# Kernel tuning notes

Measured on AMD Instinct MI355X. Metric: run time of the kernel, lower is better.

Reference implementation:

```python
import jax, jax.numpy as jnp
import numpy as np

FP = 1e-4  # floating_point smoothing constant from the source


def setup_inputs() -> dict:
    key = jax.random.key(0)
    k1, k2 = jax.random.split(key)
    N, F, B = 100000, 50, 16
    x = jax.random.randint(k1, (N, F, B), 0, 2).astype(jnp.float32)  # 0/1 one-hot-style indicators
    y = jax.random.randint(k2, (N,), 0, 2).astype(jnp.int32)         # binary labels
    return {"x": x, "y": y}


def _wls_fit(X, pct, w):
    # X: [F,K,p] design, pct: [F,K] WLS weights, w: [F,K] targets
    XtW = jnp.swapaxes(X, 1, 2) * pct[:, None, :]           # [F,p,K] = X^T W (W diagonal)
    A = XtW @ X                                              # [F,p,p]
    coef = jnp.linalg.pinv(A) @ (XtW @ w[..., None])         # [F,p,1]
    fit = (X @ coef)[..., 0]                                 # [F,K]
    return fit, coef


def reference(x, y):
    N = x.shape[0]
    m1 = (y == 1).astype(x.dtype)                            # bad mask
    m0 = (y == 0).astype(x.dtype)                            # good mask
    n1 = jnp.sum(m1)
    n0 = jnp.sum(m0)
    # per-(feature,bin) counts restricted to bad/good rows (replaces gather+reduce)
    sum_bad = jnp.einsum('nfb,n->fb', x, m1)                 # [F,B]
    sum_good = jnp.einsum('nfb,n->fb', x, m0)
    total_pct = jnp.sum(x, axis=0) / N                       # [F,B]
    woe = jnp.log(sum_bad / n1 + FP) - jnp.log(sum_good / n0 + FP)  # [F,B]

    # --- WLS adjustment on non-NaN bins (bin 0 is the NaN bin) ---
    w = woe[:, 1:]                                           # [F,K]
    pct = total_pct[:, 1:]
    pct = pct / jnp.sum(pct, axis=1, keepdims=True)
    F_, K = pct.shape
    t = jnp.arange(1, K + 1, dtype=jnp.int32)                # 1..K
    t_idx = jnp.cumsum((pct != 0).astype(jnp.int32), axis=1)
    first = jnp.argmax(t_idx == 1, axis=1).astype(jnp.int32) # first nonzero-bin position per feature
    idx = jnp.maximum(t[None, :] - first[:, None], 0).astype(x.dtype)  # [F,K]
    ind = (idx != 0).astype(x.dtype)
    X1 = jnp.stack([ind, idx], axis=2)                       # [F,K,2]
    X2 = jnp.stack([ind, idx, idx * idx], axis=2)            # [F,K,3]

    fit1, _ = _wls_fit(X1, pct, w)
    fit2, _ = _wls_fit(X2, pct, w)

    mean_w = jnp.sum(w * pct, axis=1, keepdims=True)
    sst = jnp.sum((w - mean_w) ** 2 * pct, axis=1)           # [F]
    r1 = 1 - jnp.sum((fit1 - w) ** 2 * pct, axis=1) / sst
    r2 = 1 - jnp.sum((fit2 - w) ** 2 * pct, axis=1) / sst
    adj = (fit1 * r1[:, None] + fit2 * r2[:, None]) / (r1 + r2)[:, None]
    wls_adj_woe = jnp.concatenate([woe[:, :1], adj], axis=1) # [F,B]

    # --- WOE transform of the input rows ---
    w_use = jnp.where(jnp.isnan(wls_adj_woe), 0.0, wls_adj_woe)
    rt = jnp.einsum('nfb,fb->nf', (x == 1).astype(x.dtype), w_use)  # [N,F]
    return rt, woe, wls_adj_woe
```

## Files before the change

kernel.cpp:

```cpp
#include <hip/hip_runtime.h>
#include <math.h>

#define NROWS 100000
#define NFEAT 50
#define NBINS 16
#define CELLS 5000000u

template<bool WRITE_MASK>
__global__ __launch_bounds__(256) void k1(const float* __restrict__ x,
                                          const int* __restrict__ y,
                                          float* __restrict__ part,
                                          int* __restrict__ n1part,
                                          unsigned short* __restrict__ masks) {
  const unsigned tid  = threadIdx.x;
  const unsigned gtid = blockIdx.x * 256u + tid;
  const unsigned T    = gridDim.x * 256u;
  const int f = (int)(gtid % 50u);
  float s[16], s1[16];
#pragma unroll
  for (int i = 0; i < 16; ++i) { s[i] = 0.f; s1[i] = 0.f; }
  int ycnt = 0;
  for (unsigned c = gtid; c < CELLS; c += T) {
    const float4* xc = (const float4*)(x + (size_t)c * 16u);
    float4 v0 = xc[0], v1 = xc[1], v2 = xc[2], v3 = xc[3];
    const int yy = y[c / 50u];
    float vv[16] = {v0.x, v0.y, v0.z, v0.w, v1.x, v1.y, v1.z, v1.w,
                    v2.x, v2.y, v2.z, v2.w, v3.x, v3.y, v3.z, v3.w};
    unsigned m = 0u;
#pragma unroll
    for (int b = 0; b < 16; ++b) {
      float v = vv[b];
      s[b]  += v;
      s1[b] += yy ? v : 0.0f;
      m |= (v == 1.0f ? 1u : 0u) << b;
    }
    if (WRITE_MASK) masks[c] = (unsigned short)m;
    if (f == 0) ycnt += yy;
  }
  __shared__ float lds[1600];
  __shared__ int ldsy;
  for (unsigned i = tid; i < 1600u; i += 256u) lds[i] = 0.f;
  if (tid == 0) ldsy = 0;
  __syncthreads();
#pragma unroll
  for (int b = 0; b < 16; ++b) {
    atomicAdd(&lds[f * 16 + b], s[b]);
    atomicAdd(&lds[800 + f * 16 + b], s1[b]);
  }
  if (ycnt) atomicAdd(&ldsy, ycnt);
  __syncthreads();
  float* pb = part + (size_t)blockIdx.x * 1600u;
  for (unsigned i = tid; i < 1600u; i += 256u) pb[i] = lds[i];
  if (tid == 0) n1part[blockIdx.x] = ldsy;
}

__global__ __launch_bounds__(64) void k1b(const float* __restrict__ part,
                                          float* __restrict__ finals, int nb) {
  const int i = blockIdx.x * 64 + threadIdx.x;
  float acc = 0.f;
  for (int p = 0; p < nb; ++p) acc += part[(size_t)p * 1600u + i];
  finals[i] = acc;
}

__global__ __launch_bounds__(64) void k2(const float* __restrict__ finals,
                                         const int* __restrict__ n1part, int nb,
                                         float* __restrict__ out_woe,
                                         float* __restrict__ out_adj,
                                         float* __restrict__ w_use) {
  __shared__ int sh_n1;
  const int tid = threadIdx.x;
  int cnt = 0;
  for (int p = tid; p < nb; p += 64) cnt += n1part[p];
#pragma unroll
  for (int off = 32; off > 0; off >>= 1) cnt += __shfl_down(cnt, off);
  if (tid == 0) sh_n1 = cnt;
  __syncthreads();
  if (tid >= NFEAT) return;
  const int f = tid;
  const double n1 = (double)sh_n1;
  const double n0 = (double)NROWS - n1;
  double woe[16], tp[16];
  for (int b = 0; b < 16; ++b) {
    double S  = (double)finals[f * 16 + b];
    double S1 = (double)finals[800 + f * 16 + b];
    double S0 = S - S1;
    woe[b] = log(S1 / n1 + 1e-4) - log(S0 / n0 + 1e-4);
    tp[b]  = S / (double)NROWS;
    out_woe[f * 16 + b] = (float)woe[b];
  }
  double w[15], p[15];
  double ps = 0.0;
  for (int k = 0; k < 15; ++k) { w[k] = woe[k + 1]; p[k] = tp[k + 1]; ps += p[k]; }
  for (int k = 0; k < 15; ++k) p[k] /= ps;
  int first = 0; bool found = false;
  for (int k = 0; k < 15; ++k) if (!found && p[k] != 0.0) { first = k; found = true; }
  double idx[15], ind[15];
  for (int k = 0; k < 15; ++k) {
    double t = (double)(k + 1 - first);
    idx[k] = t > 0.0 ? t : 0.0;
    ind[k] = (idx[k] != 0.0) ? 1.0 : 0.0;
  }
  double a00=0,a01=0,a02=0,a11=0,a12=0,a22=0,r0=0,r1v=0,r2v=0;
  for (int k = 0; k < 15; ++k) {
    double pi = p[k], id = idx[k], nd = ind[k], id2 = id * id;
    a00 += pi*nd*nd;  a01 += pi*nd*id;  a02 += pi*nd*id2;
    a11 += pi*id*id;  a12 += pi*id*id2; a22 += pi*id2*id2;
    r0  += pi*nd*w[k]; r1v += pi*id*w[k]; r2v += pi*id2*w[k];
  }
  double det2 = a00*a11 - a01*a01;
  double c10 = (a11*r0  - a01*r1v) / det2;
  double c11 = (a00*r1v - a01*r0 ) / det2;
  double m00 = a11*a22 - a12*a12;
  double m01 = a02*a12 - a01*a22;
  double m02 = a01*a12 - a02*a11;
  double det3 = a00*m00 + a01*m01 + a02*m02;
  double m11 = a00*a22 - a02*a02;
  double m12 = a01*a02 - a00*a12;
  double m22 = a00*a11 - a01*a01;
  double c20 = (m00*r0 + m01*r1v + m02*r2v) / det3;
  double c21 = (m01*r0 + m11*r1v + m12*r2v) / det3;
  double c22 = (m02*r0 + m12*r1v + m22*r2v) / det3;
  double mean = 0.0;
  for (int k = 0; k < 15; ++k) mean += w[k] * p[k];
  double sst = 0, sse1 = 0, sse2 = 0;
  double fit1[15], fit2[15];
  for (int k = 0; k < 15; ++k) {
    fit1[k] = ind[k]*c10 + idx[k]*c11;
    fit2[k] = ind[k]*c20 + idx[k]*c21 + idx[k]*idx[k]*c22;
    double d  = w[k] - mean;    sst  += d*d*p[k];
    double d1 = fit1[k] - w[k]; sse1 += d1*d1*p[k];
    double d2 = fit2[k] - w[k]; sse2 += d2*d2*p[k];
  }
  double R1 = 1.0 - sse1 / sst;
  double R2 = 1.0 - sse2 / sst;
  {
    float v = (float)woe[0];
    out_adj[f * 16] = v;
    w_use[f * 16] = isnan(v) ? 0.f : v;
  }
  for (int k = 0; k < 15; ++k) {
    double adj = (fit1[k]*R1 + fit2[k]*R2) / (R1 + R2);
    float v = (float)adj;
    out_adj[f * 16 + 1 + k] = v;
    w_use[f * 16 + 1 + k] = isnan(v) ? 0.f : v;
  }
}

template<bool USE_MASK>
__global__ __launch_bounds__(256) void k3(const unsigned short* __restrict__ masks,
                                          const float* __restrict__ x,
                                          const float* __restrict__ w_use,
                                          float* __restrict__ rt) {
  const unsigned gtid = blockIdx.x * 256u + threadIdx.x;
  const unsigned T    = gridDim.x * 256u;
  const int f = (int)(gtid % 50u);
  const float4* wf = (const float4*)(w_use + f * 16);
  float4 w0 = wf[0], w1 = wf[1], w2 = wf[2], w3 = wf[3];
  float wr[16] = {w0.x, w0.y, w0.z, w0.w, w1.x, w1.y, w1.z, w1.w,
                  w2.x, w2.y, w2.z, w2.w, w3.x, w3.y, w3.z, w3.w};
  for (unsigned c = gtid; c < CELLS; c += T) {
    float acc = 0.f;
    if (USE_MASK) {
      unsigned m = masks[c];
#pragma unroll
      for (int b = 0; b < 16; ++b) acc += ((m >> b) & 1u) ? wr[b] : 0.f;
    } else {
      const float4* xc = (const float4*)(x + (size_t)c * 16u);
      float4 v0 = xc[0], v1 = xc[1], v2 = xc[2], v3 = xc[3];
      float vv[16] = {v0.x, v0.y, v0.z, v0.w, v1.x, v1.y, v1.z, v1.w,
                      v2.x, v2.y, v2.z, v2.w, v3.x, v3.y, v3.z, v3.w};
#pragma unroll
      for (int b = 0; b < 16; ++b) acc += (vv[b] == 1.0f) ? wr[b] : 0.f;
    }
    rt[c] = acc;
  }
}

extern "C" void kernel_launch(void* const* d_in, const int* in_sizes, int n_in,
                              void* d_out, int out_size, void* d_ws, size_t ws_size,
                              hipStream_t stream) {
  const float* x = (const float*)d_in[0];
  const int*   y = (const int*)d_in[1];
  float* out     = (float*)d_out;
  float* rt      = out;
  float* out_woe = out + 5000000;
  float* out_adj = out + 5000800;

  auto need = [](int nb, bool mask) -> size_t {
    size_t f = (size_t)(1600 + 800 + nb) * 4 + (size_t)nb * 1600 * 4;
    if (mask) f += (size_t)CELLS * 2;
    return f + 256;
  };
  int  nb;
  bool use_mask;
  if (ws_size >= need(500, true))       { nb = 500; use_mask = true;  }
  else if (ws_size >= need(500, false)) { nb = 500; use_mask = false; }
  else                                  { nb = 25;  use_mask = false; }

  char* ws = (char*)d_ws;
  float* finals = (float*)ws;
  float* w_use  = finals + 1600;
  int*   n1part = (int*)(w_use + 800);
  float* part   = (float*)(n1part + nb);
  unsigned short* masks = (unsigned short*)(part + (size_t)nb * 1600);

  if (use_mask)
    k1<true><<<nb, 256, 0, stream>>>(x, y, part, n1part, masks);
  else
    k1<false><<<nb, 256, 0, stream>>>(x, y, part, n1part, nullptr);
  k1b<<<25, 64, 0, stream>>>(part, finals, nb);
  k2<<<1, 64, 0, stream>>>(finals, n1part, nb, out_woe, out_adj, w_use);
  if (use_mask)
    k3<true><<<2500, 256, 0, stream>>>(masks, nullptr, w_use, rt);
  else
    k3<false><<<2500, 256, 0, stream>>>(nullptr, x, w_use, rt);
}
```

Baseline: 590.5 us.

## Replace per-block partials with global atomics and widen k1 grid

```diff
diff --git a/kernel.cpp b/kernel.cpp
--- a/kernel.cpp
+++ b/kernel.cpp
@@ -5,12 +5,20 @@
 #define NFEAT 50
 #define NBINS 16
 #define CELLS 5000000u
+#define K1_BLOCKS 2500
+
+__global__ __launch_bounds__(256) void k0(float* __restrict__ finals,
+                                          int* __restrict__ n1) {
+  const int i = threadIdx.x + blockIdx.x * 256;
+  if (i < 1600) finals[i] = 0.f;
+  if (i == 0) *n1 = 0;
+}
 
 template<bool WRITE_MASK>
 __global__ __launch_bounds__(256) void k1(const float* __restrict__ x,
                                           const int* __restrict__ y,
-                                          float* __restrict__ part,
-                                          int* __restrict__ n1part,
+                                          float* __restrict__ finals,
+                                          int* __restrict__ n1,
                                           unsigned short* __restrict__ masks) {
   const unsigned tid  = threadIdx.x;
   const unsigned gtid = blockIdx.x * 256u + tid;
@@ -23,7 +31,7 @@
   for (unsigned c = gtid; c < CELLS; c += T) {
     const float4* xc = (const float4*)(x + (size_t)c * 16u);
     float4 v0 = xc[0], v1 = xc[1], v2 = xc[2], v3 = xc[3];
-    const int yy = y[c / 50u];
+    const float fy = (float)y[c / 50u];
     float vv[16] = {v0.x, v0.y, v0.z, v0.w, v1.x, v1.y, v1.z, v1.w,
                     v2.x, v2.y, v2.z, v2.w, v3.x, v3.y, v3.z, v3.w};
     unsigned m = 0u;
@@ -31,11 +39,11 @@
     for (int b = 0; b < 16; ++b) {
       float v = vv[b];
       s[b]  += v;
-      s1[b] += yy ? v : 0.0f;
+      s1[b] = fmaf(v, fy, s1[b]);
       m |= (v == 1.0f ? 1u : 0u) << b;
     }
     if (WRITE_MASK) masks[c] = (unsigned short)m;
-    if (f == 0) ycnt += yy;
+    if (f == 0) ycnt += (fy != 0.0f);
   }
   __shared__ float lds[1600];
   __shared__ int ldsy;
@@ -49,35 +57,22 @@
   }
   if (ycnt) atomicAdd(&ldsy, ycnt);
   __syncthreads();
-  float* pb = part + (size_t)blockIdx.x * 1600u;
-  for (unsigned i = tid; i < 1600u; i += 256u) pb[i] = lds[i];
-  if (tid == 0) n1part[blockIdx.x] = ldsy;
-}
-
-__global__ __launch_bounds__(64) void k1b(const float* __restrict__ part,
-                                          float* __restrict__ finals, int nb) {
-  const int i = blockIdx.x * 64 + threadIdx.x;
-  float acc = 0.f;
-  for (int p = 0; p < nb; ++p) acc += part[(size_t)p * 1600u + i];
-  finals[i] = acc;
+  for (unsigned i = tid; i < 1600u; i += 256u) {
+    float v = lds[i];
+    if (v != 0.f) atomicAdd(&finals[i], v);
+  }
+  if (tid == 0 && ldsy) atomicAdd(n1, ldsy);
 }
 
 __global__ __launch_bounds__(64) void k2(const float* __restrict__ finals,
-                                         const int* __restrict__ n1part, int nb,
+                                         const int* __restrict__ n1p,
                                          float* __restrict__ out_woe,
                                          float* __restrict__ out_adj,
                                          float* __restrict__ w_use) {
-  __shared__ int sh_n1;
   const int tid = threadIdx.x;
-  int cnt = 0;
-  for (int p = tid; p < nb; p += 64) cnt += n1part[p];
-#pragma unroll
-  for (int off = 32; off > 0; off >>= 1) cnt += __shfl_down(cnt, off);
-  if (tid == 0) sh_n1 = cnt;
-  __syncthreads();
   if (tid >= NFEAT) return;
   const int f = tid;
-  const double n1 = (double)sh_n1;
+  const double n1 = (double)(*n1p);
   const double n0 = (double)NROWS - n1;
   double woe[16], tp[16];
   for (int b = 0; b < 16; ++b) {
@@ -186,30 +181,21 @@
   float* out_woe = out + 5000000;
   float* out_adj = out + 5000800;
 
-  auto need = [](int nb, bool mask) -> size_t {
-    size_t f = (size_t)(1600 + 800 + nb) * 4 + (size_t)nb * 1600 * 4;
-    if (mask) f += (size_t)CELLS * 2;
-    return f + 256;
-  };
-  int  nb;
-  bool use_mask;
-  if (ws_size >= need(500, true))       { nb = 500; use_mask = true;  }
-  else if (ws_size >= need(500, false)) { nb = 500; use_mask = false; }
-  else                                  { nb = 25;  use_mask = false; }
-
   char* ws = (char*)d_ws;
   float* finals = (float*)ws;
-  float* w_use  = finals + 1600;
-  int*   n1part = (int*)(w_use + 800);
-  float* part   = (float*)(n1part + nb);
-  unsigned short* masks = (unsigned short*)(part + (size_t)nb * 1600);
-
+  int*   n1     = (int*)(finals + 1600);
+  float* w_use  = (float*)(n1 + 64);
+  unsigned short* masks = (unsigned short*)(w_use + 800);
+
+  const size_t base_bytes  = (size_t)(1600 + 64 + 800) * 4;
+  const bool use_mask = ws_size >= base_bytes + (size_t)CELLS * 2 + 256;
+
+  k0<<<7, 256, 0, stream>>>(finals, n1);
   if (use_mask)
-    k1<true><<<nb, 256, 0, stream>>>(x, y, part, n1part, masks);
+    k1<true><<<K1_BLOCKS, 256, 0, stream>>>(x, y, finals, n1, masks);
   else
-    k1<false><<<nb, 256, 0, stream>>>(x, y, part, n1part, nullptr);
-  k1b<<<25, 64, 0, stream>>>(part, finals, nb);
-  k2<<<1, 64, 0, stream>>>(finals, n1part, nb, out_woe, out_adj, w_use);
+    k1<false><<<K1_BLOCKS, 256, 0, stream>>>(x, y, finals, n1, nullptr);
+  k2<<<1, 64, 0, stream>>>(finals, n1, out_woe, out_adj, w_use);
   if (use_mask)
     k3<true><<<2500, 256, 0, stream>>>(masks, nullptr, w_use, rt);
   else
```

After: 505.8 us. 1.17x faster.
